# Kernel optimization log

Hardware: AMD Instinct MI355X
Metric: run time of the kernel (lower is better)

The kernel has to match this reference:

```python
import jax, jax.numpy as jnp
import numpy as np

B, T, D = 2, 2048, 2048
H = 16
HD = D // H  # 128


def _rotate_half(x):
    x1, x2 = x[..., :HD // 2], x[..., HD // 2:]
    return jnp.concatenate((-x2, x1), axis=-1)


def setup_inputs() -> dict:
    key = jax.random.key(0)
    ks = jax.random.split(key, 7)
    return {
        "x": jax.random.normal(ks[0], (B, T, D), dtype=jnp.float32),
        "rope_cos": jax.random.uniform(ks[1], (1, 1, T, HD), dtype=jnp.float32),
        "rope_sin": jax.random.uniform(ks[2], (1, 1, T, HD), dtype=jnp.float32),
        "qkv_w": jax.random.normal(ks[3], (3 * D, D), dtype=jnp.float32) * (1.0 / np.sqrt(D)),
        "qkv_b": jax.random.normal(ks[4], (3 * D,), dtype=jnp.float32) * 0.02,
        "out_w": jax.random.normal(ks[5], (D, D), dtype=jnp.float32) * (1.0 / np.sqrt(D)),
        "out_b": jax.random.normal(ks[6], (D,), dtype=jnp.float32) * 0.02,
    }


def reference(x, rope_cos, rope_sin, qkv_w, qkv_b, out_w, out_b):
    bsz, t, d = x.shape
    # fused QKV projection (torch Linear: x @ W.T + b)
    qkv = x @ qkv_w.T + qkv_b                       # [B, T, 3D]
    qkv = qkv.reshape(bsz, t, 3, H, HD).transpose(2, 0, 3, 1, 4)  # [3, B, H, T, HD]
    q, k, v = qkv[0], qkv[1], qkv[2]
    # RoPE
    cos = rope_cos[:, :, :t, :]
    sin = rope_sin[:, :, :t, :]
    q = q * cos + _rotate_half(q) * sin
    k = k * cos + _rotate_half(k) * sin
    # causal SDPA (eval mode -> no dropout)
    scale = 1.0 / np.sqrt(HD)
    scores = jnp.einsum("bhqd,bhkd->bhqk", q, k) * scale
    causal = jnp.tril(jnp.ones((t, t), dtype=bool))
    scores = jnp.where(causal, scores, jnp.finfo(scores.dtype).min)
    attn = jax.nn.softmax(scores, axis=-1)
    out = jnp.einsum("bhqk,bhkd->bhqd", attn, v)    # [B, H, T, HD]
    out = out.transpose(0, 2, 1, 3).reshape(bsz, t, d)
    return out @ out_w.T + out_b
```

## Files before the change

kernel.cpp:

```cpp
#include <hip/hip_runtime.h>

typedef unsigned short u16;
typedef __attribute__((ext_vector_type(8))) short bf16x8;
typedef __attribute__((ext_vector_type(4))) float f32x4;

__device__ __forceinline__ float bf2f(unsigned int u) {
    union { unsigned int i; float f; } x; x.i = u << 16; return x.f;
}
__device__ __forceinline__ u16 f2bf(float f) {
    union { float f; unsigned int i; } x; x.f = f;
    unsigned int r = x.i + 0x7fffu + ((x.i >> 16) & 1u);
    return (u16)(r >> 16);
}

__device__ __forceinline__ void gl2lds16(const u16* g, u16* l) {
    __builtin_amdgcn_global_load_lds(
        (const __attribute__((address_space(1))) unsigned int*)g,
        (__attribute__((address_space(3))) unsigned int*)l, 16, 0, 0);
}

#define NX  8388608
#define NW1 12582912
#define NW2 4194304
__global__ __launch_bounds__(256) void convert_kernel(
    const float* __restrict__ x, const float* __restrict__ w1,
    const float* __restrict__ w2, u16* __restrict__ dst)
{
    const int i = (blockIdx.x * 256 + threadIdx.x) * 4;
    const float* src;
    int off;
    if (i < NX)            { src = x;  off = i; }
    else if (i < NX + NW1) { src = w1; off = i - NX; }
    else                   { src = w2; off = i - NX - NW1; }
    float4 v = *(const float4*)(src + off);
    ushort4 o;
    o.x = f2bf(v.x); o.y = f2bf(v.y); o.z = f2bf(v.z); o.w = f2bf(v.w);
    *(ushort4*)(dst + i) = o;
}

#define NTILES 64
#define BUFSZ  12288

#define GEMM_SETUP(Ag, Bg)                                                    \
    const int tid = threadIdx.x;                                              \
    const int wave = tid >> 6, lane = tid & 63;                               \
    const int l16 = lane & 15, quad = lane >> 4;                              \
    const int wr = wave >> 2, wc = wave & 3;                                  \
    f32x4 acc[4][4];                                                          \
    _Pragma("unroll") for (int mi = 0; mi < 4; ++mi)                          \
        _Pragma("unroll") for (int ni = 0; ni < 4; ++ni)                      \
            acc[mi][ni] = (f32x4){0.f, 0.f, 0.f, 0.f};                        \
    int aoff[4], boff[4];                                                     \
    _Pragma("unroll") for (int mi = 0; mi < 4; ++mi) {                        \
        const int r = wr * 64 + mi * 16 + l16;                                \
        aoff[mi] = r * 32 + ((quad ^ ((r >> 1) & 3)) << 3);                   \
    }                                                                         \
    _Pragma("unroll") for (int ni = 0; ni < 4; ++ni) {                        \
        const int r = (wc >> 1) * 128 + (ni >> 1) * 64 + (wc & 1) * 32        \
                    + (ni & 1) * 16 + l16;                                    \
        boff[ni] = 4096 + r * 32 + ((quad ^ ((r >> 1) & 3)) << 3);            \
    }                                                                         \
    const u16* sbase[3]; int sdst[3];                                         \
    _Pragma("unroll") for (int j = 0; j < 3; ++j) {                           \
        const int c = wave * 3 + j;                                           \
        const int g = lane & 3;                                               \
        int r; const u16* bp; int d;                                          \
        if (c < 8) {                                                          \
            r = c * 16 + (lane >> 2);                                         \
            bp = Ag + (size_t)(m0 + r) * 2048;                                \
            d = c * 512 + lane * 8;                                           \
        } else {                                                              \
            r = (c - 8) * 16 + (lane >> 2);                                   \
            bp = Bg + (size_t)(n0 + r) * 2048;                                \
            d = 4096 + (c - 8) * 512 + lane * 8;                              \
        }                                                                     \
        sbase[j] = bp + ((g ^ ((r >> 1) & 3)) << 3);                          \
        sdst[j] = d;                                                          \
    }                                                                         \
          \
    _Pragma("unroll") for (int pt = 0; pt < 5; ++pt)                          \
        _Pragma("unroll") for (int j = 0; j < 3; ++j)                         \
            gl2lds16(sbase[j] + pt * 32, lds + pt * BUFSZ + sdst[j]);         \
    bf16x8 afr[2][4], bfr[2][4];                                              \
    asm volatile("s_waitcnt vmcnt(9)" ::: "memory");                          \
    __builtin_amdgcn_s_barrier();                                             \
    _Pragma("unroll") for (int mi = 0; mi < 4; ++mi)                          \
        afr[0][mi] = *(const bf16x8*)(lds + aoff[mi]);                        \
    _Pragma("unroll") for (int ni = 0; ni < 4; ++ni)                          \
        bfr[0][ni] = *(const bf16x8*)(lds + boff[ni]);

#define GEMM_PHASE(T, P, STAGE, VM, LOADNEXT)                                 \
    {                                                                         \
        if (STAGE) {                                                          \
            u16* nbuf = lds + sw * BUFSZ;                                     \
            _Pragma("unroll") for (int j = 0; j < 3; ++j)                     \
                gl2lds16(sbase[j] + ((T) + 5) * 32, nbuf + sdst[j]);          \
        }                                                                     \
        asm volatile("s_waitcnt vmcnt(" #VM ")" ::: "memory");                \
        asm volatile("s_waitcnt lgkmcnt(0)" ::: "memory");                    \
        __builtin_amdgcn_sched_barrier(0);                                    \
        __builtin_amdgcn_s_setprio(1);                                        \
        _Pragma("unroll") for (int mi = 0; mi < 2; ++mi)                      \
            _Pragma("unroll") for (int ni = 0; ni < 4; ++ni)                  \
                acc[mi][ni] = __builtin_amdgcn_mfma_f32_16x16x32_bf16(        \
                    afr[P][mi], bfr[P][ni], acc[mi][ni], 0, 0, 0);            \
        if (LOADNEXT) {                                                       \
            const u16* rb = lds + sr * BUFSZ;                                 \
            _Pragma("unroll") for (int mi = 0; mi < 4; ++mi)                  \
                afr[(P) ^ 1][mi] = *(const bf16x8*)(rb + aoff[mi]);           \
            _Pragma("unroll") for (int ni = 0; ni < 4; ++ni)                  \
                bfr[(P) ^ 1][ni] = *(const bf16x8*)(rb + boff[ni]);           \
        }                                                                     \
        _Pragma("unroll") for (int mi = 2; mi < 4; ++mi)                      \
            _Pragma("unroll") for (int ni = 0; ni < 4; ++ni)                  \
                acc[mi][ni] = __builtin_amdgcn_mfma_f32_16x16x32_bf16(        \
                    afr[P][mi], bfr[P][ni], acc[mi][ni], 0, 0, 0);            \
        __builtin_amdgcn_s_setprio(0);                                        \
        __builtin_amdgcn_sched_barrier(0);                                    \
        __builtin_amdgcn_s_barrier();                                         \
        sr = (sr == 5) ? 0 : sr + 1;                                          \
        sw = (sw == 5) ? 0 : sw + 1;                                          \
    }

#define GEMM_MAIN()                                                           \
    int sr = 1, sw = 5;                                                       \
    for (int t = 0; t < 58; t += 2) {                                         \
        GEMM_PHASE(t,     0, 1, 9, 1)                                         \
        GEMM_PHASE(t + 1, 1, 1, 9, 1)                                         \
    }                                                                         \
    GEMM_PHASE(58, 0, 1, 9, 1)                                                \
    GEMM_PHASE(59, 1, 0, 6, 1)                                                \
    GEMM_PHASE(60, 0, 0, 3, 1)                                                \
    GEMM_PHASE(61, 1, 0, 0, 1)                                                \
    GEMM_PHASE(62, 0, 0, 0, 1)                                                \
    GEMM_PHASE(63, 1, 0, 0, 0)

__global__ __launch_bounds__(512, 2) void qkv8_kernel(
    const u16* __restrict__ xb, const u16* __restrict__ wb,
    const float* __restrict__ bias, const float* __restrict__ rc,
    const float* __restrict__ rs, u16* __restrict__ Qo,
    u16* __restrict__ Ko, u16* __restrict__ Vo)
{
    __shared__ u16 lds[6 * BUFSZ];
    const int bid = blockIdx.x;
    const int swz = (bid & 7) * 96 + (bid >> 3);
    const int m0 = (swz & 31) * 128;
    const int n0 = (swz >> 5) * 256;

    GEMM_SETUP(xb, wb)
    GEMM_MAIN()

    const int e  = n0 >> 11;
    const int h  = ((n0 & 2047) >> 7) + (wc >> 1);
    const int hb = n0 + (wc >> 1) * 128;
    const int hq = wc & 1;
    if (e < 2) {
        u16* dst = (e == 0) ? Qo : Ko;
        #pragma unroll
        for (int mi = 0; mi < 4; ++mi) {
            #pragma unroll
            for (int r = 0; r < 4; ++r) {
                const int m = m0 + wr * 64 + mi * 16 + quad * 4 + r;
                const int b = m >> 11, tt = m & 2047;
                u16* drow = dst + ((size_t)(b * 16 + h) * 2048 + tt) * 128;
                const float* crow = rc + tt * 128;
                const float* sr2  = rs + tt * 128;
                #pragma unroll
                for (int p = 0; p < 2; ++p) {
                    const int hd1 = hq * 32 + p * 16 + l16;
                    const int hd2 = hd1 + 64;
                    const float v1 = acc[mi][p][r]     + bias[hb + hd1];
                    const float v2 = acc[mi][p + 2][r] + bias[hb + hd2];
                    drow[hd1] = f2bf(v1 * crow[hd1] - v2 * sr2[hd1]);
                    drow[hd2] = f2bf(v2 * crow[hd2] + v1 * sr2[hd2]);
                }
            }
        }
    } else {
        #pragma unroll
        for (int mi = 0; mi < 4; ++mi) {
            const int mb = m0 + wr * 64 + mi * 16 + quad * 4;
            const int b = mb >> 11, tt = mb & 2047;
            u16* vbase = Vo + (size_t)(b * 16 + h) * 128 * 2048 + tt;
            #pragma unroll
            for (int ni = 0; ni < 4; ++ni) {
                const int hd = (ni >> 1) * 64 + hq * 32 + (ni & 1) * 16 + l16;
                const float bs = bias[hb + hd];
                ushort4 o;
                #pragma unroll
                for (int r = 0; r < 4; ++r)
                    ((u16*)&o)[r] = f2bf(acc[mi][ni][r] + bs);
                *(ushort4*)(vbase + (size_t)hd * 2048) = o;
            }
        }
    }
}

#define KPAD 136
#define VPAD 72
#define PPAD 72

__global__ __launch_bounds__(256) void attn_mfma_kernel(
    const u16* __restrict__ Qi, const u16* __restrict__ Ki,
    const u16* __restrict__ Vg, u16* __restrict__ Oo)
{
    __shared__ u16 Ks[64 * KPAD];
    __shared__ u16 Vt[128 * VPAD];
    __shared__ u16 Ps[4][16 * PPAD];

    const int tid  = threadIdx.x;
    const int wave = tid >> 6, lane = tid & 63;
    const int l16 = lane & 15, quad = lane >> 4;
    const int bh = blockIdx.y;
    const size_t base = (size_t)bh * (2048 * 128);

    const int qtile[2] = { (int)blockIdx.x, 31 - (int)blockIdx.x };

    bf16x8 qf[2][4];
    f32x4 o[2][8];
    float l_i[2][4];
    #pragma unroll
    for (int s = 0; s < 2; ++s) {
        const u16* qp = Qi + base + (size_t)(qtile[s] * 64 + wave * 16 + l16) * 128 + quad * 8;
        #pragma unroll
        for (int c = 0; c < 4; ++c) qf[s][c] = *(const bf16x8*)(qp + c * 32);
        #pragma unroll
        for (int i = 0; i < 8; ++i) o[s][i] = (f32x4){0.f, 0.f, 0.f, 0.f};
        #pragma unroll
        for (int r = 0; r < 4; ++r) l_i[s][r] = 0.f;
    }

    const float scale = 0.08838834764831845f;
    const int ntiles = qtile[1] + 1;

    for (int t = 0; t < ntiles; ++t) {
        const int kt = t * 64;
        __syncthreads();
        {
            const int key = tid >> 2, d0 = (tid & 3) * 32;
            const u16* src = Ki + base + (size_t)(kt + key) * 128 + d0;
            u16* dst = Ks + key * KPAD + d0;
            #pragma unroll
            for (int i = 0; i < 4; ++i)
                *(bf16x8*)(dst + 8 * i) = *(const bf16x8*)(src + 8 * i);
        }
        {
            const int d = tid >> 1, koff = (tid & 1) * 32;
            const u16* src = Vg + ((size_t)bh * 128 + d) * 2048 + kt + koff;
            u16* dst = Vt + d * VPAD + koff;
            #pragma unroll
            for (int i = 0; i < 4; ++i)
                *(bf16x8*)(dst + 8 * i) = *(const bf16x8*)(src + 8 * i);
        }
        __syncthreads();

        const bool act_a = (t <= qtile[0]);

        f32x4 sa[4], sb[4];
        #pragma unroll
        for (int nt = 0; nt < 4; ++nt) {
            sa[nt] = (f32x4){0.f, 0.f, 0.f, 0.f};
            sb[nt] = (f32x4){0.f, 0.f, 0.f, 0.f};
            #pragma unroll
            for (int c = 0; c < 4; ++c) {
                bf16x8 kf = *(const bf16x8*)(Ks + (nt * 16 + l16) * KPAD + c * 32 + quad * 8);
                sb[nt] = __builtin_amdgcn_mfma_f32_16x16x32_bf16(qf[1][c], kf, sb[nt], 0, 0, 0);
                sa[nt] = __builtin_amdgcn_mfma_f32_16x16x32_bf16(qf[0][c], kf, sa[nt], 0, 0, 0);
            }
        }

        #pragma unroll
        for (int s = 0; s < 2; ++s) {
            if (s == 0 && !act_a) continue;
            f32x4* sc = (s == 0) ? sa : sb;
            const int qrow = qtile[s] * 64 + wave * 16 + quad * 4;
            const bool diag = (t == qtile[s]);

            #pragma unroll
            for (int nt = 0; nt < 4; ++nt) {
                #pragma unroll
                for (int r = 0; r < 4; ++r) {
                    float v = sc[nt][r] * scale - 11.0f;
                    if (diag) {
                        const int key = kt + nt * 16 + l16;
                        v = (key <= qrow + r) ? v : -1.0e30f;
                    }
                    const float e = __expf(v);
                    sc[nt][r] = e;
                    l_i[s][r] += e;
                }
            }

            u16* pw = Ps[wave];
            #pragma unroll
            for (int nt = 0; nt < 4; ++nt)
                #pragma unroll
                for (int r = 0; r < 4; ++r)
                    pw[(quad * 4 + r) * PPAD + nt * 16 + l16] = f2bf(sc[nt][r]);

            bf16x8 pf0 = *(const bf16x8*)(pw + l16 * PPAD + quad * 8);
            bf16x8 pf1 = *(const bf16x8*)(pw + l16 * PPAD + 32 + quad * 8);

            #pragma unroll
            for (int nt = 0; nt < 8; ++nt) {
                bf16x8 vf0 = *(const bf16x8*)(Vt + (nt * 16 + l16) * VPAD + quad * 8);
                bf16x8 vf1 = *(const bf16x8*)(Vt + (nt * 16 + l16) * VPAD + 32 + quad * 8);
                o[s][nt] = __builtin_amdgcn_mfma_f32_16x16x32_bf16(pf0, vf0, o[s][nt], 0, 0, 0);
                o[s][nt] = __builtin_amdgcn_mfma_f32_16x16x32_bf16(pf1, vf1, o[s][nt], 0, 0, 0);
            }
        }
    }

    const int b = bh >> 4, h = bh & 15;
    #pragma unroll
    for (int s = 0; s < 2; ++s) {
        const int qrow = qtile[s] * 64 + wave * 16 + quad * 4;
        #pragma unroll
        for (int r = 0; r < 4; ++r) {
            float ls = l_i[s][r];
            ls += __shfl_xor(ls, 1, 16);
            ls += __shfl_xor(ls, 2, 16);
            ls += __shfl_xor(ls, 4, 16);
            ls += __shfl_xor(ls, 8, 16);
            const float inv = 1.f / ls;
            u16* orow = Oo + ((size_t)(b * 2048 + qrow + r)) * 2048 + h * 128 + l16;
            #pragma unroll
            for (int nt = 0; nt < 8; ++nt)
                orow[nt * 16] = f2bf(o[s][nt][r] * inv);
        }
    }
}

__global__ __launch_bounds__(512, 2) void proj8_kernel(
    const u16* __restrict__ A, const u16* __restrict__ wb,
    const float* __restrict__ bias, float* __restrict__ out)
{
    __shared__ u16 lds[6 * BUFSZ];
    const int bid = blockIdx.x;
    const int swz = (bid & 7) * 32 + (bid >> 3);
    const int m0 = (swz & 31) * 128;
    const int n0 = (swz >> 5) * 256;

    GEMM_SETUP(A, wb)
    GEMM_MAIN()

    #pragma unroll
    for (int mi = 0; mi < 4; ++mi) {
        #pragma unroll
        for (int r = 0; r < 4; ++r) {
            const int m = m0 + wr * 64 + mi * 16 + quad * 4 + r;
            float* orow = out + (size_t)m * 2048;
            #pragma unroll
            for (int ni = 0; ni < 4; ++ni) {
                const int n = n0 + (wc >> 1) * 128 + (ni >> 1) * 64
                            + (wc & 1) * 32 + (ni & 1) * 16 + l16;
                orow[n] = acc[mi][ni][r] + bias[n];
            }
        }
    }
}

extern "C" void kernel_launch(void* const* d_in, const int* in_sizes, int n_in,
                              void* d_out, int out_size, void* d_ws, size_t ws_size,
                              hipStream_t stream) {
    const float* x     = (const float*)d_in[0];
    const float* rcos  = (const float*)d_in[1];
    const float* rsin  = (const float*)d_in[2];
    const float* qkv_w = (const float*)d_in[3];
    const float* qkv_b = (const float*)d_in[4];
    const float* out_w = (const float*)d_in[5];
    const float* out_b = (const float*)d_in[6];
    float* out = (float*)d_out;

    const size_t NE = (size_t)2 * 16 * 2048 * 128;
    u16* Q      = (u16*)d_ws;
    u16* K      = Q + NE;
    u16* V      = K + NE;
    u16* xb     = V + NE;
    u16* O      = xb;
    u16* qkv_wb = xb + NX;
    u16* out_wb = qkv_wb + NW1;

    convert_kernel<<<dim3((NX + NW1 + NW2) / 1024), 256, 0, stream>>>(
        x, qkv_w, out_w, xb);
    qkv8_kernel<<<dim3(768), 512, 0, stream>>>(
        xb, qkv_wb, qkv_b, rcos, rsin, Q, K, V);
    attn_mfma_kernel<<<dim3(16, 32), 256, 0, stream>>>(Q, K, V, O);
    proj8_kernel<<<dim3(256), 512, 0, stream>>>(O, out_wb, out_b, out);
}
```

Measured before the change: 380.8 us.

## Shrink GEMM LDS ring to four stages and reschedule fragment reads before MFMAs

The QKV and output-projection GEMMs now use a 4-slot LDS ring with 3 tiles in flight instead of a 6-slot ring with 5, cutting shared memory per block by a third. Each phase now waits on global loads, barriers, issues the next fragment's LDS reads, then runs all 16 MFMAs. Before, the reads were interleaved between the two halves of the MFMA block. The smaller LDS footprint may help occupancy or cache pressure, but there is less prefetch depth to hide global latency and the extra barrier per phase adds synchronisation.

```diff
diff --git a/kernel.cpp b/kernel.cpp
--- a/kernel.cpp
+++ b/kernel.cpp
@@ -77,63 +77,58 @@
         sbase[j] = bp + ((g ^ ((r >> 1) & 3)) << 3);                          \
         sdst[j] = d;                                                          \
     }                                                                         \
-          \
-    _Pragma("unroll") for (int pt = 0; pt < 5; ++pt)                          \
+       \
+    _Pragma("unroll") for (int pt = 0; pt < 3; ++pt)                          \
         _Pragma("unroll") for (int j = 0; j < 3; ++j)                         \
             gl2lds16(sbase[j] + pt * 32, lds + pt * BUFSZ + sdst[j]);         \
     bf16x8 afr[2][4], bfr[2][4];                                              \
-    asm volatile("s_waitcnt vmcnt(9)" ::: "memory");                          \
+    asm volatile("s_waitcnt vmcnt(6)" ::: "memory");                          \
     __builtin_amdgcn_s_barrier();                                             \
     _Pragma("unroll") for (int mi = 0; mi < 4; ++mi)                          \
         afr[0][mi] = *(const bf16x8*)(lds + aoff[mi]);                        \
     _Pragma("unroll") for (int ni = 0; ni < 4; ++ni)                          \
         bfr[0][ni] = *(const bf16x8*)(lds + boff[ni]);
 
-#define GEMM_PHASE(T, P, STAGE, VM, LOADNEXT)                                 \
+#define GPH(TT, SLOT, PAR, STG, VMN, RD, LGN)                                 \
     {                                                                         \
-        if (STAGE) {                                                          \
-            u16* nbuf = lds + sw * BUFSZ;                                     \
+        if (STG) {                                                            \
+            u16* nb = lds + (((SLOT) + 3) & 3) * BUFSZ;                       \
             _Pragma("unroll") for (int j = 0; j < 3; ++j)                     \
-                gl2lds16(sbase[j] + ((T) + 5) * 32, nbuf + sdst[j]);          \
+                gl2lds16(sbase[j] + ((TT) + 3) * 32, nb + sdst[j]);           \
         }                                                                     \
-        asm volatile("s_waitcnt vmcnt(" #VM ")" ::: "memory");                \
-        asm volatile("s_waitcnt lgkmcnt(0)" ::: "memory");                    \
+        asm volatile("s_waitcnt vmcnt(" #VMN ")" ::: "memory");               \
+        __builtin_amdgcn_s_barrier();                                         \
+        if (RD) {                                                             \
+            const u16* rb = lds + (((SLOT) + 1) & 3) * BUFSZ;                 \
+            _Pragma("unroll") for (int mi = 0; mi < 4; ++mi)                  \
+                afr[(PAR) ^ 1][mi] = *(const bf16x8*)(rb + aoff[mi]);         \
+            _Pragma("unroll") for (int ni = 0; ni < 4; ++ni)                  \
+                bfr[(PAR) ^ 1][ni] = *(const bf16x8*)(rb + boff[ni]);         \
+        }                                                                     \
+        asm volatile("s_waitcnt lgkmcnt(" #LGN ")" ::: "memory");             \
         __builtin_amdgcn_sched_barrier(0);                                    \
         __builtin_amdgcn_s_setprio(1);                                        \
-        _Pragma("unroll") for (int mi = 0; mi < 2; ++mi)                      \
+        _Pragma("unroll") for (int mi = 0; mi < 4; ++mi)                      \
             _Pragma("unroll") for (int ni = 0; ni < 4; ++ni)                  \
                 acc[mi][ni] = __builtin_amdgcn_mfma_f32_16x16x32_bf16(        \
-                    afr[P][mi], bfr[P][ni], acc[mi][ni], 0, 0, 0);            \
-        if (LOADNEXT) {                                                       \
-            const u16* rb = lds + sr * BUFSZ;                                 \
-            _Pragma("unroll") for (int mi = 0; mi < 4; ++mi)                  \
-                afr[(P) ^ 1][mi] = *(const bf16x8*)(rb + aoff[mi]);           \
-            _Pragma("unroll") for (int ni = 0; ni < 4; ++ni)                  \
-                bfr[(P) ^ 1][ni] = *(const bf16x8*)(rb + boff[ni]);           \
-        }                                                                     \
-        _Pragma("unroll") for (int mi = 2; mi < 4; ++mi)                      \
-            _Pragma("unroll") for (int ni = 0; ni < 4; ++ni)                  \
-                acc[mi][ni] = __builtin_amdgcn_mfma_f32_16x16x32_bf16(        \
-                    afr[P][mi], bfr[P][ni], acc[mi][ni], 0, 0, 0);            \
+                    afr[PAR][mi], bfr[PAR][ni], acc[mi][ni], 0, 0, 0);        \
         __builtin_amdgcn_s_setprio(0);                                        \
         __builtin_amdgcn_sched_barrier(0);                                    \
         __builtin_amdgcn_s_barrier();                                         \
-        sr = (sr == 5) ? 0 : sr + 1;                                          \
-        sw = (sw == 5) ? 0 : sw + 1;                                          \
     }
 
 #define GEMM_MAIN()                                                           \
-    int sr = 1, sw = 5;                                                       \
-    for (int t = 0; t < 58; t += 2) {                                         \
-        GEMM_PHASE(t,     0, 1, 9, 1)                                         \
-        GEMM_PHASE(t + 1, 1, 1, 9, 1)                                         \
+    for (int t = 0; t < 15; ++t) {                                            \
+        const int T = t * 4;                                                  \
+        GPH(T,     0, 0, 1, 6, 1, 8)                                          \
+        GPH(T + 1, 1, 1, 1, 6, 1, 8)                                          \
+        GPH(T + 2, 2, 0, 1, 6, 1, 8)                                          \
+        GPH(T + 3, 3, 1, 1, 6, 1, 8)                                          \
     }                                                                         \
-    GEMM_PHASE(58, 0, 1, 9, 1)                                                \
-    GEMM_PHASE(59, 1, 0, 6, 1)                                                \
-    GEMM_PHASE(60, 0, 0, 3, 1)                                                \
-    GEMM_PHASE(61, 1, 0, 0, 1)                                                \
-    GEMM_PHASE(62, 0, 0, 0, 1)                                                \
-    GEMM_PHASE(63, 1, 0, 0, 0)
+    GPH(60, 0, 0, 1, 6, 1, 8)                                                 \
+    GPH(61, 1, 1, 0, 3, 1, 8)                                                 \
+    GPH(62, 2, 0, 0, 0, 1, 8)                                                 \
+    GPH(63, 3, 1, 0, 0, 0, 0)
 
 __global__ __launch_bounds__(512, 2) void qkv8_kernel(
     const u16* __restrict__ xb, const u16* __restrict__ wb,
@@ -141,7 +136,7 @@
     const float* __restrict__ rs, u16* __restrict__ Qo,
     u16* __restrict__ Ko, u16* __restrict__ Vo)
 {
-    __shared__ u16 lds[6 * BUFSZ];
+    __shared__ u16 lds[4 * BUFSZ];
     const int bid = blockIdx.x;
     const int swz = (bid & 7) * 96 + (bid >> 3);
     const int m0 = (swz & 31) * 128;
@@ -335,7 +330,7 @@
     const u16* __restrict__ A, const u16* __restrict__ wb,
     const float* __restrict__ bias, float* __restrict__ out)
 {
-    __shared__ u16 lds[6 * BUFSZ];
+    __shared__ u16 lds[4 * BUFSZ];
     const int bid = blockIdx.x;
     const int swz = (bid & 7) * 32 + (bid >> 3);
     const int m0 = (swz & 31) * 128;
```

New measurement: 380.4 us. Within noise of the previous version (-0.1%).
